# Optimization experiments

Measured on AMD Instinct MI355X. Metric: run time of the kernel, lower is better.

Reference implementation:

```python
import jax, jax.numpy as jnp
import numpy as np


def maxpool2x2(x):
    # NCHW 2x2 max pool, stride 2
    return jax.lax.reduce_window(x, -jnp.inf, jax.lax.max, (1, 1, 2, 2), (1, 1, 2, 2), 'VALID')


def _xavier_uniform(k, shape):
    fan_out, fan_in = shape
    lim = np.sqrt(6.0 / (fan_in + fan_out))
    return jax.random.uniform(k, shape, jnp.float32, -lim, lim)


def setup_inputs() -> dict:
    key = jax.random.key(0)
    ks = jax.random.split(key, 5)
    C = 64
    x = jax.random.normal(ks[0], (4, C, 128, 128), jnp.float32)
    Wq = _xavier_uniform(ks[1], (C // 8, C))  # 1x1 conv == channel matmul
    Wk = _xavier_uniform(ks[2], (C // 8, C))
    Wv = _xavier_uniform(ks[3], (C // 2, C))
    Wo = _xavier_uniform(ks[4], (C, C // 2))
    gamma = jnp.full((1,), 0.1, jnp.float32)  # nonzero so attention branch contributes
    return {"x": x, "Wq": Wq, "Wk": Wk, "Wv": Wv, "Wo": Wo, "gamma": gamma}


def reference(x, Wq, Wk, Wv, Wo, gamma):
    b, c, w, h = x.shape
    # 1x1 convs as channel contractions
    q = jnp.einsum('oc,bchw->bohw', Wq, x).reshape(b, c // 8, w * h)          # [b, c/8, k]
    k_ = maxpool2x2(jnp.einsum('oc,bchw->bohw', Wk, x)).reshape(b, c // 8, -1)  # [b, c/8, f]
    v = maxpool2x2(jnp.einsum('oc,bchw->bohw', Wv, x)).reshape(b, c // 2, -1)   # [b, c/2, f]
    # softmax over full-resolution query positions k (last axis), per pooled position f
    weights = jax.nn.softmax(jnp.einsum('bcf,bck->bfk', k_, q), axis=-1)        # [b, f, k]
    out = jnp.einsum('bcf,bfk->bck', v, weights).reshape(b, c // 2, w, h)       # [b, c/2, w, h]
    out = jnp.einsum('oc,bchw->bohw', Wo, out)                                   # [b, c, w, h]
    return gamma * out + x
```

## Files before the change

kernel.cpp:

```cpp
#include <hip/hip_runtime.h>
#include <cstdint>
#include <cstddef>


#define LOG2E 1.44269504088896340736f

typedef __attribute__((ext_vector_type(8)))  __bf16 bf8_t;
typedef __attribute__((ext_vector_type(16))) float  fx16;

__device__ __forceinline__ unsigned short f2bf(float f) {
  unsigned int u = __builtin_bit_cast(unsigned int, f);
  u += 0x7FFFu + ((u >> 16) & 1u);
  return (unsigned short)(u >> 16);
}
__device__ __forceinline__ unsigned int pk2(unsigned short lo, unsigned short hi) {
  return (unsigned int)lo | ((unsigned int)hi << 16);
}
__device__ __forceinline__ int pi16(int s) {
  int m = (s >> 2) & 3;
  return (m == 1 || m == 2) ? (s ^ 12) : s;
}
__device__ __forceinline__ float max4(const float* a) {
  return fmaxf(fmaxf(a[0], a[1]), fmaxf(a[2], a[3]));
}

#if __has_builtin(__builtin_amdgcn_exp2f)
#define EXP2F __builtin_amdgcn_exp2f
#else
#define EXP2F exp2f
#endif

__global__ void __launch_bounds__(256) k_qkv(const float* __restrict__ x,
                                             const float* __restrict__ Wq,
                                             const float* __restrict__ Wk,
                                             const float* __restrict__ Wv,
                                             const float* __restrict__ Wo,
                                             unsigned short* __restrict__ Qp,
                                             unsigned short* __restrict__ KpB,
                                             float* __restrict__ Vp,
                                             unsigned short* __restrict__ Wop) {
  if (blockIdx.x == 256) {
    for (int i = threadIdx.x; i < 2048; i += 256) {
      int c = i & 31;
      Wop[i] = f2bf(Wo[(i & ~31) | (c & 16) | pi16(c & 15)]);
    }
    return;
  }
  __shared__ float ws[48][64];
  __shared__ float xs[16][256];
  int t = threadIdx.x;
  for (int i = t; i < 512; i += 256) {
    ws[i >> 6][i & 63] = Wq[i];
    ws[8 + (i >> 6)][i & 63] = Wk[i];
  }
  for (int i = t; i < 2048; i += 256) ws[16 + (i >> 6)][i & 63] = Wv[i];
  int b = blockIdx.x >> 6, frow = blockIdx.x & 63;
  int rg = t >> 6, fc = t & 63;
  const float* xb = x + (size_t)b * (64 * 16384) + frow * 256;
  float acc[12][4];
#pragma unroll
  for (int j = 0; j < 12; ++j)
#pragma unroll
    for (int p = 0; p < 4; ++p) acc[j][p] = 0.f;
  int cl = t >> 4, seg = t & 15;
  for (int cc = 0; cc < 4; ++cc) {
    __syncthreads();
    const float4* src =
        reinterpret_cast<const float4*>(xb + (size_t)(cc * 16 + cl) * 16384 + seg * 16);
    float4* dst = reinterpret_cast<float4*>(&xs[cl][seg * 16]);
#pragma unroll
    for (int j = 0; j < 4; ++j) dst[j] = src[j];
    __syncthreads();
#pragma unroll
    for (int c16 = 0; c16 < 16; ++c16) {
      int c = cc * 16 + c16;
      float2 xa = *reinterpret_cast<const float2*>(&xs[c16][2 * fc]);
      float2 xbv = *reinterpret_cast<const float2*>(&xs[c16][128 + 2 * fc]);
#pragma unroll
      for (int j = 0; j < 12; ++j) {
        float w = ws[12 * rg + j][c];
        acc[j][0] = fmaf(w, xa.x, acc[j][0]);
        acc[j][1] = fmaf(w, xa.y, acc[j][1]);
        acc[j][2] = fmaf(w, xbv.x, acc[j][2]);
        acc[j][3] = fmaf(w, xbv.y, acc[j][3]);
      }
    }
  }
  size_t idx = (size_t)b * 4096 + frow * 64 + fc;
  uint4 z4; z4.x = z4.y = z4.z = z4.w = 0u;
  if (rg == 0) {
#pragma unroll
    for (int p = 0; p < 4; ++p) {
      int kpos = frow * 256 + (p >> 1) * 128 + 2 * fc + (p & 1);
      uint4 qa;
      qa.x = pk2(f2bf(acc[0][p]), f2bf(acc[1][p]));
      qa.y = pk2(f2bf(acc[2][p]), f2bf(acc[3][p]));
      qa.z = pk2(f2bf(acc[4][p]), f2bf(acc[5][p]));
      qa.w = pk2(f2bf(acc[6][p]), f2bf(acc[7][p]));
      uint4* qdst = reinterpret_cast<uint4*>(Qp + ((size_t)b * 16384 + kpos) * 16);
      qdst[0] = qa; qdst[1] = z4;
    }
    uint2 kw;
    kw.x = pk2(f2bf(max4(acc[8]) * LOG2E), f2bf(max4(acc[9]) * LOG2E));
    kw.y = pk2(f2bf(max4(acc[10]) * LOG2E), f2bf(max4(acc[11]) * LOG2E));
    *reinterpret_cast<uint2*>(KpB + idx * 16) = kw;
  } else if (rg == 1) {
    uint2 kw;
    kw.x = pk2(f2bf(max4(acc[0]) * LOG2E), f2bf(max4(acc[1]) * LOG2E));
    kw.y = pk2(f2bf(max4(acc[2]) * LOG2E), f2bf(max4(acc[3]) * LOG2E));
    *reinterpret_cast<uint2*>(KpB + idx * 16 + 4) = kw;
    *reinterpret_cast<uint4*>(KpB + idx * 16 + 8) = z4;
    float* vd = Vp + idx * 32;
    *reinterpret_cast<float4*>(vd) =
        make_float4(max4(acc[4]), max4(acc[5]), max4(acc[6]), max4(acc[7]));
    *reinterpret_cast<float4*>(vd + 4) =
        make_float4(max4(acc[8]), max4(acc[9]), max4(acc[10]), max4(acc[11]));
  } else {
    float* vd = Vp + idx * 32 + (rg == 2 ? 8 : 20);
#pragma unroll
    for (int j4 = 0; j4 < 3; ++j4)
      *reinterpret_cast<float4*>(vd + 4 * j4) =
          make_float4(max4(acc[4 * j4]), max4(acc[4 * j4 + 1]),
                      max4(acc[4 * j4 + 2]), max4(acc[4 * j4 + 3]));
  }
}

__global__ void __launch_bounds__(1024) k_lsum(const unsigned short* __restrict__ Qp,
                                               const unsigned short* __restrict__ KpB,
                                               const float* __restrict__ Vp,
                                               unsigned short* __restrict__ Vpp) {
  int b = blockIdx.x >> 6, g = blockIdx.x & 63;
  int wv = threadIdx.x >> 6, lane = threadIdx.x & 63;
  int half = lane >> 5, l31 = lane & 31;
  const unsigned short* kb =
      KpB + ((size_t)(b * 4096 + g * 64 + l31)) * 16 + half * 8;
  bf8_t A0 = *reinterpret_cast<const bf8_t*>(kb);
  bf8_t A1 = *reinterpret_cast<const bf8_t*>(kb + 32 * 16);
  const unsigned short* qbase = Qp + ((size_t)b * 16384) * 16 + half * 8;
  fx16 z;
#pragma unroll
  for (int i = 0; i < 16; ++i) z[i] = 0.f;
  float l[32];
#pragma unroll
  for (int i = 0; i < 32; ++i) l[i] = 0.f;
  int t0 = wv * 32;
  bf8_t B = *reinterpret_cast<const bf8_t*>(qbase + (size_t)(t0 * 32 + l31) * 16);
  for (int i = 0; i < 32; ++i) {
    int tn = t0 + ((i + 1) & 31);
    bf8_t nB = *reinterpret_cast<const bf8_t*>(qbase + (size_t)(tn * 32 + l31) * 16);
    fx16 s0 = __builtin_amdgcn_mfma_f32_32x32x16_bf16(A0, B, z, 0, 0, 0);
    fx16 s1 = __builtin_amdgcn_mfma_f32_32x32x16_bf16(A1, B, z, 0, 0, 0);
#pragma unroll
    for (int r0 = 0; r0 < 16; ++r0) l[r0] += EXP2F(s0[r0]);
#pragma unroll
    for (int r0 = 0; r0 < 16; ++r0) l[16 + r0] += EXP2F(s1[r0]);
    B = nB;
  }
#pragma unroll
  for (int r0 = 0; r0 < 32; ++r0)
    for (int d = 1; d < 32; d <<= 1) l[r0] += __shfl_xor(l[r0], d);
  __shared__ float sl[16][2][32];
  __shared__ float Linv[64];
  __shared__ unsigned short Tv[32][72];
  if (l31 == 0) {
#pragma unroll
    for (int r0 = 0; r0 < 16; ++r0) {
      int row = (r0 & 3) + 8 * (r0 >> 2) + 4 * half;
      sl[wv][0][row] = l[r0];
      sl[wv][1][row] = l[16 + r0];
    }
  }
  __syncthreads();
  if (threadIdx.x < 64) {
    int fgi = threadIdx.x >> 5, row = threadIdx.x & 31;
    float L = 0.f;
#pragma unroll
    for (int w2 = 0; w2 < 16; ++w2) L += sl[w2][fgi][row];
    Linv[threadIdx.x] = 1.0f / L;
  }
  __syncthreads();
  if (threadIdx.x < 512) {
    int floc = threadIdx.x >> 3, c4 = (threadIdx.x & 7) * 4;
    float4 v = *reinterpret_cast<const float4*>(
        Vp + ((size_t)(b * 4096 + g * 64 + floc)) * 32 + c4);
    float s = Linv[floc];
    int dst = (floc & ~15) | pi16(floc & 15);
    Tv[c4][dst]     = f2bf(v.x * s);
    Tv[c4 + 1][dst] = f2bf(v.y * s);
    Tv[c4 + 2][dst] = f2bf(v.z * s);
    Tv[c4 + 3][dst] = f2bf(v.w * s);
  }
  __syncthreads();
  if (threadIdx.x < 256) {
    int c = threadIdx.x >> 3, u = threadIdx.x & 7;
    uint4 val = *reinterpret_cast<const uint4*>(&Tv[c][u * 8]);
    *reinterpret_cast<uint4*>(Vpp + ((size_t)(b * 32 + c)) * 4096 + g * 64 + u * 8) = val;
  }
}

__global__ void __launch_bounds__(512) k_attn(const unsigned short* __restrict__ Qp,
                                              const unsigned short* __restrict__ KpB,
                                              const unsigned short* __restrict__ Vpp,
                                              const unsigned short* __restrict__ Wop,
                                              const float* __restrict__ x,
                                              const float* __restrict__ gamma,
                                              float* __restrict__ out) {
  int b = blockIdx.x >> 8, kp = blockIdx.x & 255;
  int wv = threadIdx.x >> 6, lane = threadIdx.x & 63;
  int half = lane >> 5, l31 = lane & 31;
  int kbase = kp * 64;
  const unsigned short* qb = Qp + ((size_t)b * 16384 + kbase + l31) * 16 + half * 8;
  bf8_t Bq0 = *reinterpret_cast<const bf8_t*>(qb);
  bf8_t Bq1 = *reinterpret_cast<const bf8_t*>(qb + 32 * 16);
  fx16 z;
#pragma unroll
  for (int i = 0; i < 16; ++i) z[i] = 0.f;
  fx16 acc0 = z, acc1 = z;
  const unsigned short* kpB = KpB + ((size_t)b * 4096 + l31) * 16 + half * 8;
  const unsigned short* vpB = Vpp + ((size_t)(b * 32 + l31)) * 4096 + half * 8;
  int c0 = wv * 16;
  int f0 = c0 * 32;
  bf8_t Ak  = *reinterpret_cast<const bf8_t*>(kpB + (size_t)f0 * 16);
  bf8_t Av0 = *reinterpret_cast<const bf8_t*>(vpB + f0);
  bf8_t Av1 = *reinterpret_cast<const bf8_t*>(vpB + f0 + 16);
  for (int fc = 0; fc < 16; ++fc) {
    int f1 = (c0 + ((fc + 1) & 15)) * 32;
    bf8_t nAk  = *reinterpret_cast<const bf8_t*>(kpB + (size_t)f1 * 16);
    bf8_t nAv0 = *reinterpret_cast<const bf8_t*>(vpB + f1);
    bf8_t nAv1 = *reinterpret_cast<const bf8_t*>(vpB + f1 + 16);
    fx16 s0 = __builtin_amdgcn_mfma_f32_32x32x16_bf16(Ak, Bq0, z, 0, 0, 0);
    fx16 s1 = __builtin_amdgcn_mfma_f32_32x32x16_bf16(Ak, Bq1, z, 0, 0, 0);
    bf8_t P00, P01, P10, P11;
#pragma unroll
    for (int j = 0; j < 8; ++j) {
      P00[j] = (__bf16)EXP2F(s0[j]);
      P01[j] = (__bf16)EXP2F(s0[8 + j]);
    }
#pragma unroll
    for (int j = 0; j < 8; ++j) {
      P10[j] = (__bf16)EXP2F(s1[j]);
      P11[j] = (__bf16)EXP2F(s1[8 + j]);
    }
    acc0 = __builtin_amdgcn_mfma_f32_32x32x16_bf16(Av0, P00, acc0, 0, 0, 0);
    acc1 = __builtin_amdgcn_mfma_f32_32x32x16_bf16(Av0, P10, acc1, 0, 0, 0);
    acc0 = __builtin_amdgcn_mfma_f32_32x32x16_bf16(Av1, P01, acc0, 0, 0, 0);
    acc1 = __builtin_amdgcn_mfma_f32_32x32x16_bf16(Av1, P11, acc1, 0, 0, 0);
    Ak = nAk; Av0 = nAv0; Av1 = nAv1;
  }
  __shared__ float sacc[4][2][4][64][4];
  if (wv >= 4) {
    int s = wv - 4;
#pragma unroll
    for (int j4 = 0; j4 < 4; ++j4) {
      *reinterpret_cast<float4*>(&sacc[s][0][j4][lane][0]) =
          make_float4(acc0[4 * j4], acc0[4 * j4 + 1], acc0[4 * j4 + 2], acc0[4 * j4 + 3]);
      *reinterpret_cast<float4*>(&sacc[s][1][j4][lane][0]) =
          make_float4(acc1[4 * j4], acc1[4 * j4 + 1], acc1[4 * j4 + 2], acc1[4 * j4 + 3]);
    }
  }
  __syncthreads();
  if (wv < 4) {
#pragma unroll
    for (int j4 = 0; j4 < 4; ++j4) {
      float4 p0 = *reinterpret_cast<const float4*>(&sacc[wv][0][j4][lane][0]);
      float4 p1 = *reinterpret_cast<const float4*>(&sacc[wv][1][j4][lane][0]);
      p0.x += acc0[4 * j4]; p0.y += acc0[4 * j4 + 1];
      p0.z += acc0[4 * j4 + 2]; p0.w += acc0[4 * j4 + 3];
      p1.x += acc1[4 * j4]; p1.y += acc1[4 * j4 + 1];
      p1.z += acc1[4 * j4 + 2]; p1.w += acc1[4 * j4 + 3];
      *reinterpret_cast<float4*>(&sacc[wv][0][j4][lane][0]) = p0;
      *reinterpret_cast<float4*>(&sacc[wv][1][j4][lane][0]) = p1;
    }
  }
  __syncthreads();
  if (wv >= 4) return;
  int kt = wv & 1, ot = wv >> 1;
  fx16 tot;
#pragma unroll
  for (int j4 = 0; j4 < 4; ++j4) {
    float4 a0 = *reinterpret_cast<const float4*>(&sacc[0][kt][j4][lane][0]);
    float4 a1 = *reinterpret_cast<const float4*>(&sacc[1][kt][j4][lane][0]);
    float4 a2 = *reinterpret_cast<const float4*>(&sacc[2][kt][j4][lane][0]);
    float4 a3 = *reinterpret_cast<const float4*>(&sacc[3][kt][j4][lane][0]);
    tot[4 * j4]     = (a0.x + a1.x) + (a2.x + a3.x);
    tot[4 * j4 + 1] = (a0.y + a1.y) + (a2.y + a3.y);
    tot[4 * j4 + 2] = (a0.z + a1.z) + (a2.z + a3.z);
    tot[4 * j4 + 3] = (a0.w + a1.w) + (a2.w + a3.w);
  }
  bf8_t Ob0, Ob1;
#pragma unroll
  for (int j = 0; j < 8; ++j) { Ob0[j] = (__bf16)tot[j]; Ob1[j] = (__bf16)tot[8 + j]; }
  const unsigned short* wb = Wop + (ot * 32 + l31) * 32 + half * 8;
  bf8_t Aw0 = *reinterpret_cast<const bf8_t*>(wb);
  bf8_t Aw1 = *reinterpret_cast<const bf8_t*>(wb + 16);
  fx16 y = __builtin_amdgcn_mfma_f32_32x32x16_bf16(Aw0, Ob0, z, 0, 0, 0);
  y = __builtin_amdgcn_mfma_f32_32x32x16_bf16(Aw1, Ob1, y, 0, 0, 0);
  float g = gamma[0];
  int k = kbase + kt * 32 + l31;
  const float* xp = x + (size_t)b * 64 * 16384 + k;
  float* op = out + (size_t)b * 64 * 16384 + k;
#pragma unroll
  for (int r0 = 0; r0 < 16; ++r0) {
    int row = (r0 & 3) + 8 * (r0 >> 2) + 4 * half + ot * 32;
    op[(size_t)row * 16384] = fmaf(g, y[r0], xp[(size_t)row * 16384]);
  }
}

extern "C" void kernel_launch(void* const* d_in, const int* in_sizes, int n_in,
                              void* d_out, int out_size, void* d_ws, size_t ws_size,
                              hipStream_t stream) {
  const float* x     = (const float*)d_in[0];
  const float* Wq    = (const float*)d_in[1];
  const float* Wk    = (const float*)d_in[2];
  const float* Wv    = (const float*)d_in[3];
  const float* Wo    = (const float*)d_in[4];
  const float* gamma = (const float*)d_in[5];
  float* out = (float*)d_out;
  char* ws = (char*)d_ws;
  unsigned short* Qp  = (unsigned short*)(ws + 0);
  unsigned short* KpB = (unsigned short*)(ws + 2097152);
  float*          Vp  = (float*)(ws + 2621440);
  unsigned short* Vpp = (unsigned short*)(ws + 4718592);
  unsigned short* Wop = (unsigned short*)(ws + 5767168);

  k_qkv <<<dim3(257),  dim3(256),  0, stream>>>(x, Wq, Wk, Wv, Wo, Qp, KpB, Vp, Wop);
  k_lsum<<<dim3(256),  dim3(1024), 0, stream>>>(Qp, KpB, Vp, Vpp);
  k_attn<<<dim3(1024), dim3(512),  0, stream>>>(Qp, KpB, Vpp, Wop, x, gamma, out);
}
```

Measured before the change: 149.8 us.

## Use bit-trick exp2, split row-sum kernel, remap QKV projection threads

Replaces hardware exp2 with a Schraudolph-style integer bit-cast approximation that packs directly into bf16 in the attention loop and in the softmax denominator pass. The row-sum kernel is split across two key halves for more blocks, and V normalisation and packing move to a separate kernel. The QKV projection uses 512 threads, with 2x2 pooling done via lane shuffles and transposed weights read as float4. The attention epilogue prefetches the residual x before the reduction and drops one barrier. The exp approximation lowers accuracy of the softmax weights, and the extra kernel launch adds overhead.

```diff
diff --git a/kernel.cpp b/kernel.cpp
--- a/kernel.cpp
+++ b/kernel.cpp
@@ -4,6 +4,8 @@
 
 
 #define LOG2E 1.44269504088896340736f
+#define FE_A 8388608.0f
+#define FE_B 1064993098.0f
 
 typedef __attribute__((ext_vector_type(8)))  __bf16 bf8_t;
 typedef __attribute__((ext_vector_type(16))) float  fx16;
@@ -20,17 +22,17 @@
   int m = (s >> 2) & 3;
   return (m == 1 || m == 2) ? (s ^ 12) : s;
 }
-__device__ __forceinline__ float max4(const float* a) {
-  return fmaxf(fmaxf(a[0], a[1]), fmaxf(a[2], a[3]));
-}
-
-#if __has_builtin(__builtin_amdgcn_exp2f)
-#define EXP2F __builtin_amdgcn_exp2f
-#else
-#define EXP2F exp2f
-#endif
-
-__global__ void __launch_bounds__(256) k_qkv(const float* __restrict__ x,
+__device__ __forceinline__ unsigned fe_u(float s) {
+  return (unsigned)fmaf(s, FE_A, FE_B);
+}
+__device__ __forceinline__ float fe_f(float s) {
+  return __builtin_bit_cast(float, fe_u(s));
+}
+__device__ __forceinline__ unsigned fe_pk(float s0, float s1) {
+  return __builtin_amdgcn_perm(fe_u(s1), fe_u(s0), 0x07060302);
+}
+
+__global__ void __launch_bounds__(512) k_qkv(const float* __restrict__ x,
                                              const float* __restrict__ Wq,
                                              const float* __restrict__ Wk,
                                              const float* __restrict__ Wv,
@@ -40,58 +42,64 @@
                                              float* __restrict__ Vp,
                                              unsigned short* __restrict__ Wop) {
   if (blockIdx.x == 256) {
-    for (int i = threadIdx.x; i < 2048; i += 256) {
+    for (int i = threadIdx.x; i < 2048; i += 512) {
       int c = i & 31;
       Wop[i] = f2bf(Wo[(i & ~31) | (c & 16) | pi16(c & 15)]);
     }
     return;
   }
-  __shared__ float ws[48][64];
+  __shared__ float wst[64][48];
   __shared__ float xs[16][256];
   int t = threadIdx.x;
-  for (int i = t; i < 512; i += 256) {
-    ws[i >> 6][i & 63] = Wq[i];
-    ws[8 + (i >> 6)][i & 63] = Wk[i];
-  }
-  for (int i = t; i < 2048; i += 256) ws[16 + (i >> 6)][i & 63] = Wv[i];
+  for (int i = t; i < 512; i += 512) {
+    wst[i & 63][i >> 6] = Wq[i];
+    wst[i & 63][8 + (i >> 6)] = Wk[i];
+  }
+  for (int i = t; i < 2048; i += 512) wst[i & 63][16 + (i >> 6)] = Wv[i];
   int b = blockIdx.x >> 6, frow = blockIdx.x & 63;
-  int rg = t >> 6, fc = t & 63;
+  int wvx = t >> 6, rg = wvx & 3, h = wvx >> 2;
+  int lane = t & 63, c2 = lane >> 1, cpos = lane & 1;
+  int cell = h * 32 + c2, col = h * 64 + lane;
   const float* xb = x + (size_t)b * (64 * 16384) + frow * 256;
-  float acc[12][4];
-#pragma unroll
-  for (int j = 0; j < 12; ++j)
-#pragma unroll
-    for (int p = 0; p < 4; ++p) acc[j][p] = 0.f;
-  int cl = t >> 4, seg = t & 15;
+  float acc[12][2];
+#pragma unroll
+  for (int j = 0; j < 12; ++j) { acc[j][0] = 0.f; acc[j][1] = 0.f; }
+  int cl = t >> 5, seg = t & 31;
   for (int cc = 0; cc < 4; ++cc) {
     __syncthreads();
     const float4* src =
-        reinterpret_cast<const float4*>(xb + (size_t)(cc * 16 + cl) * 16384 + seg * 16);
-    float4* dst = reinterpret_cast<float4*>(&xs[cl][seg * 16]);
-#pragma unroll
-    for (int j = 0; j < 4; ++j) dst[j] = src[j];
+        reinterpret_cast<const float4*>(xb + (size_t)(cc * 16 + cl) * 16384 + seg * 8);
+    float4* dst = reinterpret_cast<float4*>(&xs[cl][seg * 8]);
+    dst[0] = src[0]; dst[1] = src[1];
     __syncthreads();
 #pragma unroll
     for (int c16 = 0; c16 < 16; ++c16) {
       int c = cc * 16 + c16;
-      float2 xa = *reinterpret_cast<const float2*>(&xs[c16][2 * fc]);
-      float2 xbv = *reinterpret_cast<const float2*>(&xs[c16][128 + 2 * fc]);
+      float xa = xs[c16][col], xo = xs[c16][128 + col];
+      float4 w0 = *reinterpret_cast<const float4*>(&wst[c][12 * rg]);
+      float4 w1 = *reinterpret_cast<const float4*>(&wst[c][12 * rg + 4]);
+      float4 w2 = *reinterpret_cast<const float4*>(&wst[c][12 * rg + 8]);
+      float wj[12] = {w0.x, w0.y, w0.z, w0.w, w1.x, w1.y, w1.z, w1.w,
+                      w2.x, w2.y, w2.z, w2.w};
 #pragma unroll
       for (int j = 0; j < 12; ++j) {
-        float w = ws[12 * rg + j][c];
-        acc[j][0] = fmaf(w, xa.x, acc[j][0]);
-        acc[j][1] = fmaf(w, xa.y, acc[j][1]);
-        acc[j][2] = fmaf(w, xbv.x, acc[j][2]);
-        acc[j][3] = fmaf(w, xbv.y, acc[j][3]);
+        acc[j][0] = fmaf(wj[j], xa, acc[j][0]);
+        acc[j][1] = fmaf(wj[j], xo, acc[j][1]);
       }
     }
   }
-  size_t idx = (size_t)b * 4096 + frow * 64 + fc;
+  float pm[12];
+#pragma unroll
+  for (int j = 0; j < 12; ++j) {
+    pm[j] = fmaxf(acc[j][0], acc[j][1]);
+    pm[j] = fmaxf(pm[j], __shfl_xor(pm[j], 1));
+  }
+  size_t idx = (size_t)b * 4096 + frow * 64 + cell;
   uint4 z4; z4.x = z4.y = z4.z = z4.w = 0u;
   if (rg == 0) {
 #pragma unroll
-    for (int p = 0; p < 4; ++p) {
-      int kpos = frow * 256 + (p >> 1) * 128 + 2 * fc + (p & 1);
+    for (int p = 0; p < 2; ++p) {
+      int kpos = frow * 256 + p * 128 + col;
       uint4 qa;
       qa.x = pk2(f2bf(acc[0][p]), f2bf(acc[1][p]));
       qa.y = pk2(f2bf(acc[2][p]), f2bf(acc[3][p]));
@@ -100,101 +108,94 @@
       uint4* qdst = reinterpret_cast<uint4*>(Qp + ((size_t)b * 16384 + kpos) * 16);
       qdst[0] = qa; qdst[1] = z4;
     }
-    uint2 kw;
-    kw.x = pk2(f2bf(max4(acc[8]) * LOG2E), f2bf(max4(acc[9]) * LOG2E));
-    kw.y = pk2(f2bf(max4(acc[10]) * LOG2E), f2bf(max4(acc[11]) * LOG2E));
-    *reinterpret_cast<uint2*>(KpB + idx * 16) = kw;
+    if (cpos == 0) {
+      uint2 kw;
+      kw.x = pk2(f2bf(pm[8] * LOG2E), f2bf(pm[9] * LOG2E));
+      kw.y = pk2(f2bf(pm[10] * LOG2E), f2bf(pm[11] * LOG2E));
+      *reinterpret_cast<uint2*>(KpB + idx * 16) = kw;
+    }
   } else if (rg == 1) {
-    uint2 kw;
-    kw.x = pk2(f2bf(max4(acc[0]) * LOG2E), f2bf(max4(acc[1]) * LOG2E));
-    kw.y = pk2(f2bf(max4(acc[2]) * LOG2E), f2bf(max4(acc[3]) * LOG2E));
-    *reinterpret_cast<uint2*>(KpB + idx * 16 + 4) = kw;
-    *reinterpret_cast<uint4*>(KpB + idx * 16 + 8) = z4;
-    float* vd = Vp + idx * 32;
-    *reinterpret_cast<float4*>(vd) =
-        make_float4(max4(acc[4]), max4(acc[5]), max4(acc[6]), max4(acc[7]));
-    *reinterpret_cast<float4*>(vd + 4) =
-        make_float4(max4(acc[8]), max4(acc[9]), max4(acc[10]), max4(acc[11]));
-  } else {
+    if (cpos == 0) {
+      uint2 kw;
+      kw.x = pk2(f2bf(pm[0] * LOG2E), f2bf(pm[1] * LOG2E));
+      kw.y = pk2(f2bf(pm[2] * LOG2E), f2bf(pm[3] * LOG2E));
+      *reinterpret_cast<uint2*>(KpB + idx * 16 + 4) = kw;
+      *reinterpret_cast<uint4*>(KpB + idx * 16 + 8) = z4;
+      float* vd = Vp + idx * 32;
+      *reinterpret_cast<float4*>(vd) = make_float4(pm[4], pm[5], pm[6], pm[7]);
+      *reinterpret_cast<float4*>(vd + 4) = make_float4(pm[8], pm[9], pm[10], pm[11]);
+    }
+  } else if (cpos == 0) {
     float* vd = Vp + idx * 32 + (rg == 2 ? 8 : 20);
 #pragma unroll
     for (int j4 = 0; j4 < 3; ++j4)
       *reinterpret_cast<float4*>(vd + 4 * j4) =
-          make_float4(max4(acc[4 * j4]), max4(acc[4 * j4 + 1]),
-                      max4(acc[4 * j4 + 2]), max4(acc[4 * j4 + 3]));
+          make_float4(pm[4 * j4], pm[4 * j4 + 1], pm[4 * j4 + 2], pm[4 * j4 + 3]);
   }
 }
 
 __global__ void __launch_bounds__(1024) k_lsum(const unsigned short* __restrict__ Qp,
                                                const unsigned short* __restrict__ KpB,
-                                               const float* __restrict__ Vp,
-                                               unsigned short* __restrict__ Vpp) {
-  int b = blockIdx.x >> 6, g = blockIdx.x & 63;
+                                               float* __restrict__ Lpart) {
+  int b = blockIdx.x >> 8, r = blockIdx.x & 255;
+  int fg = r >> 1, kh = r & 1;
   int wv = threadIdx.x >> 6, lane = threadIdx.x & 63;
   int half = lane >> 5, l31 = lane & 31;
-  const unsigned short* kb =
-      KpB + ((size_t)(b * 4096 + g * 64 + l31)) * 16 + half * 8;
-  bf8_t A0 = *reinterpret_cast<const bf8_t*>(kb);
-  bf8_t A1 = *reinterpret_cast<const bf8_t*>(kb + 32 * 16);
+  bf8_t A = *reinterpret_cast<const bf8_t*>(
+      KpB + ((size_t)(b * 4096 + fg * 32 + l31)) * 16 + half * 8);
   const unsigned short* qbase = Qp + ((size_t)b * 16384) * 16 + half * 8;
   fx16 z;
 #pragma unroll
   for (int i = 0; i < 16; ++i) z[i] = 0.f;
-  float l[32];
-#pragma unroll
-  for (int i = 0; i < 32; ++i) l[i] = 0.f;
-  int t0 = wv * 32;
+  float l[16];
+#pragma unroll
+  for (int i = 0; i < 16; ++i) l[i] = 0.f;
+  int t0 = kh * 256 + wv * 16;
   bf8_t B = *reinterpret_cast<const bf8_t*>(qbase + (size_t)(t0 * 32 + l31) * 16);
-  for (int i = 0; i < 32; ++i) {
-    int tn = t0 + ((i + 1) & 31);
+  for (int i = 0; i < 16; ++i) {
+    int tn = t0 + ((i + 1) & 15);
     bf8_t nB = *reinterpret_cast<const bf8_t*>(qbase + (size_t)(tn * 32 + l31) * 16);
-    fx16 s0 = __builtin_amdgcn_mfma_f32_32x32x16_bf16(A0, B, z, 0, 0, 0);
-    fx16 s1 = __builtin_amdgcn_mfma_f32_32x32x16_bf16(A1, B, z, 0, 0, 0);
-#pragma unroll
-    for (int r0 = 0; r0 < 16; ++r0) l[r0] += EXP2F(s0[r0]);
-#pragma unroll
-    for (int r0 = 0; r0 < 16; ++r0) l[16 + r0] += EXP2F(s1[r0]);
+    fx16 s = __builtin_amdgcn_mfma_f32_32x32x16_bf16(A, B, z, 0, 0, 0);
+#pragma unroll
+    for (int r0 = 0; r0 < 16; ++r0) l[r0] += fe_f(s[r0]);
     B = nB;
   }
 #pragma unroll
-  for (int r0 = 0; r0 < 32; ++r0)
+  for (int r0 = 0; r0 < 16; ++r0)
     for (int d = 1; d < 32; d <<= 1) l[r0] += __shfl_xor(l[r0], d);
-  __shared__ float sl[16][2][32];
-  __shared__ float Linv[64];
-  __shared__ unsigned short Tv[32][72];
+  __shared__ float sl[16][32];
   if (l31 == 0) {
 #pragma unroll
     for (int r0 = 0; r0 < 16; ++r0) {
       int row = (r0 & 3) + 8 * (r0 >> 2) + 4 * half;
-      sl[wv][0][row] = l[r0];
-      sl[wv][1][row] = l[16 + r0];
+      sl[wv][row] = l[r0];
     }
   }
   __syncthreads();
-  if (threadIdx.x < 64) {
-    int fgi = threadIdx.x >> 5, row = threadIdx.x & 31;
+  if (threadIdx.x < 32) {
     float L = 0.f;
 #pragma unroll
-    for (int w2 = 0; w2 < 16; ++w2) L += sl[w2][fgi][row];
-    Linv[threadIdx.x] = 1.0f / L;
-  }
+    for (int w2 = 0; w2 < 16; ++w2) L += sl[w2][threadIdx.x];
+    Lpart[(size_t)kh * 16384 + b * 4096 + fg * 32 + threadIdx.x] = L;
+  }
+}
+
+__global__ void __launch_bounds__(256) k_pack(const float* __restrict__ Vp,
+                                              const float* __restrict__ Lpart,
+                                              unsigned short* __restrict__ Vpp) {
+  int b = blockIdx.x >> 4, f0 = (blockIdx.x & 15) * 256;
+  __shared__ unsigned short T[32][264];
+  int t = threadIdx.x;
+  size_t li = (size_t)b * 4096 + f0 + t;
+  float rl = 1.0f / (Lpart[li] + Lpart[16384 + li]);
+  const float* vp = Vp + li * 32;
+  int fl = (t & ~15) | pi16(t & 15);
+  for (int c = 0; c < 32; ++c) T[c][fl] = f2bf(vp[c] * rl);
   __syncthreads();
-  if (threadIdx.x < 512) {
-    int floc = threadIdx.x >> 3, c4 = (threadIdx.x & 7) * 4;
-    float4 v = *reinterpret_cast<const float4*>(
-        Vp + ((size_t)(b * 4096 + g * 64 + floc)) * 32 + c4);
-    float s = Linv[floc];
-    int dst = (floc & ~15) | pi16(floc & 15);
-    Tv[c4][dst]     = f2bf(v.x * s);
-    Tv[c4 + 1][dst] = f2bf(v.y * s);
-    Tv[c4 + 2][dst] = f2bf(v.z * s);
-    Tv[c4 + 3][dst] = f2bf(v.w * s);
-  }
-  __syncthreads();
-  if (threadIdx.x < 256) {
-    int c = threadIdx.x >> 3, u = threadIdx.x & 7;
-    uint4 val = *reinterpret_cast<const uint4*>(&Tv[c][u * 8]);
-    *reinterpret_cast<uint4*>(Vpp + ((size_t)(b * 32 + c)) * 4096 + g * 64 + u * 8) = val;
+  for (int u = t; u < 1024; u += 256) {
+    int row = u >> 5, e0 = (u & 31) * 8;
+    uint4 val = *reinterpret_cast<const uint4*>(&T[row][e0]);
+    *reinterpret_cast<uint4*>(Vpp + ((size_t)b * 32 + row) * 4096 + f0 + e0) = val;
   }
 }
 
@@ -230,17 +231,19 @@
     bf8_t nAv1 = *reinterpret_cast<const bf8_t*>(vpB + f1 + 16);
     fx16 s0 = __builtin_amdgcn_mfma_f32_32x32x16_bf16(Ak, Bq0, z, 0, 0, 0);
     fx16 s1 = __builtin_amdgcn_mfma_f32_32x32x16_bf16(Ak, Bq1, z, 0, 0, 0);
-    bf8_t P00, P01, P10, P11;
-#pragma unroll
-    for (int j = 0; j < 8; ++j) {
-      P00[j] = (__bf16)EXP2F(s0[j]);
-      P01[j] = (__bf16)EXP2F(s0[8 + j]);
-    }
-#pragma unroll
-    for (int j = 0; j < 8; ++j) {
-      P10[j] = (__bf16)EXP2F(s1[j]);
-      P11[j] = (__bf16)EXP2F(s1[8 + j]);
-    }
+    uint4 u00, u01, u10, u11;
+    u00.x = fe_pk(s0[0], s0[1]);   u00.y = fe_pk(s0[2], s0[3]);
+    u00.z = fe_pk(s0[4], s0[5]);   u00.w = fe_pk(s0[6], s0[7]);
+    u01.x = fe_pk(s0[8], s0[9]);   u01.y = fe_pk(s0[10], s0[11]);
+    u01.z = fe_pk(s0[12], s0[13]); u01.w = fe_pk(s0[14], s0[15]);
+    u10.x = fe_pk(s1[0], s1[1]);   u10.y = fe_pk(s1[2], s1[3]);
+    u10.z = fe_pk(s1[4], s1[5]);   u10.w = fe_pk(s1[6], s1[7]);
+    u11.x = fe_pk(s1[8], s1[9]);   u11.y = fe_pk(s1[10], s1[11]);
+    u11.z = fe_pk(s1[12], s1[13]); u11.w = fe_pk(s1[14], s1[15]);
+    bf8_t P00 = __builtin_bit_cast(bf8_t, u00);
+    bf8_t P01 = __builtin_bit_cast(bf8_t, u01);
+    bf8_t P10 = __builtin_bit_cast(bf8_t, u10);
+    bf8_t P11 = __builtin_bit_cast(bf8_t, u11);
     acc0 = __builtin_amdgcn_mfma_f32_32x32x16_bf16(Av0, P00, acc0, 0, 0, 0);
     acc1 = __builtin_amdgcn_mfma_f32_32x32x16_bf16(Av0, P10, acc1, 0, 0, 0);
     acc0 = __builtin_amdgcn_mfma_f32_32x32x16_bf16(Av1, P01, acc0, 0, 0, 0);
@@ -259,22 +262,28 @@
     }
   }
   __syncthreads();
-  if (wv < 4) {
-#pragma unroll
-    for (int j4 = 0; j4 < 4; ++j4) {
-      float4 p0 = *reinterpret_cast<const float4*>(&sacc[wv][0][j4][lane][0]);
-      float4 p1 = *reinterpret_cast<const float4*>(&sacc[wv][1][j4][lane][0]);
-      p0.x += acc0[4 * j4]; p0.y += acc0[4 * j4 + 1];
-      p0.z += acc0[4 * j4 + 2]; p0.w += acc0[4 * j4 + 3];
-      p1.x += acc1[4 * j4]; p1.y += acc1[4 * j4 + 1];
-      p1.z += acc1[4 * j4 + 2]; p1.w += acc1[4 * j4 + 3];
-      *reinterpret_cast<float4*>(&sacc[wv][0][j4][lane][0]) = p0;
-      *reinterpret_cast<float4*>(&sacc[wv][1][j4][lane][0]) = p1;
-    }
-  }
-  __syncthreads();
   if (wv >= 4) return;
   int kt = wv & 1, ot = wv >> 1;
+  int k = kbase + kt * 32 + l31;
+  const float* xp = x + (size_t)b * 64 * 16384 + k;
+  float xv[16];
+#pragma unroll
+  for (int r0 = 0; r0 < 16; ++r0) {
+    int row = (r0 & 3) + 8 * (r0 >> 2) + 4 * half + ot * 32;
+    xv[r0] = xp[(size_t)row * 16384];
+  }
+#pragma unroll
+  for (int j4 = 0; j4 < 4; ++j4) {
+    float4 p0 = *reinterpret_cast<const float4*>(&sacc[wv][0][j4][lane][0]);
+    float4 p1 = *reinterpret_cast<const float4*>(&sacc[wv][1][j4][lane][0]);
+    p0.x += acc0[4 * j4]; p0.y += acc0[4 * j4 + 1];
+    p0.z += acc0[4 * j4 + 2]; p0.w += acc0[4 * j4 + 3];
+    p1.x += acc1[4 * j4]; p1.y += acc1[4 * j4 + 1];
+    p1.z += acc1[4 * j4 + 2]; p1.w += acc1[4 * j4 + 3];
+    *reinterpret_cast<float4*>(&sacc[wv][0][j4][lane][0]) = p0;
+    *reinterpret_cast<float4*>(&sacc[wv][1][j4][lane][0]) = p1;
+  }
+  __syncthreads();
   fx16 tot;
 #pragma unroll
   for (int j4 = 0; j4 < 4; ++j4) {
@@ -296,13 +305,11 @@
   fx16 y = __builtin_amdgcn_mfma_f32_32x32x16_bf16(Aw0, Ob0, z, 0, 0, 0);
   y = __builtin_amdgcn_mfma_f32_32x32x16_bf16(Aw1, Ob1, y, 0, 0, 0);
   float g = gamma[0];
-  int k = kbase + kt * 32 + l31;
-  const float* xp = x + (size_t)b * 64 * 16384 + k;
   float* op = out + (size_t)b * 64 * 16384 + k;
 #pragma unroll
   for (int r0 = 0; r0 < 16; ++r0) {
     int row = (r0 & 3) + 8 * (r0 >> 2) + 4 * half + ot * 32;
-    op[(size_t)row * 16384] = fmaf(g, y[r0], xp[(size_t)row * 16384]);
+    op[(size_t)row * 16384] = fmaf(g, y[r0], xv[r0]);
   }
 }
 
@@ -317,13 +324,15 @@
   const float* gamma = (const float*)d_in[5];
   float* out = (float*)d_out;
   char* ws = (char*)d_ws;
-  unsigned short* Qp  = (unsigned short*)(ws + 0);
-  unsigned short* KpB = (unsigned short*)(ws + 2097152);
-  float*          Vp  = (float*)(ws + 2621440);
-  unsigned short* Vpp = (unsigned short*)(ws + 4718592);
-  unsigned short* Wop = (unsigned short*)(ws + 5767168);
-
-  k_qkv <<<dim3(257),  dim3(256),  0, stream>>>(x, Wq, Wk, Wv, Wo, Qp, KpB, Vp, Wop);
-  k_lsum<<<dim3(256),  dim3(1024), 0, stream>>>(Qp, KpB, Vp, Vpp);
+  unsigned short* Qp    = (unsigned short*)(ws + 0);
+  unsigned short* KpB   = (unsigned short*)(ws + 2097152);
+  float*          Vp    = (float*)(ws + 2621440);
+  unsigned short* Vpp   = (unsigned short*)(ws + 4718592);
+  float*          Lpart = (float*)(ws + 5767168);
+  unsigned short* Wop   = (unsigned short*)(ws + 5898240);
+
+  k_qkv <<<dim3(257),  dim3(512),  0, stream>>>(x, Wq, Wk, Wv, Wo, Qp, KpB, Vp, Wop);
+  k_lsum<<<dim3(1024), dim3(1024), 0, stream>>>(Qp, KpB, Lpart);
+  k_pack<<<dim3(64),   dim3(256),  0, stream>>>(Vp, Lpart, Vpp);
   k_attn<<<dim3(1024), dim3(512),  0, stream>>>(Qp, KpB, Vpp, Wop, x, gamma, out);
 }
```

New measurement: 154.0 us. 2.7% more time.
